# Kernel optimization log

Measured on AMD Instinct MI355X. Metric: run time of the kernel, lower is better.

Reference implementation:

```python
import jax, jax.numpy as jnp
import numpy as np

N, K, G, E, OUT = 50000, 32, 512, 400000, 8
EPS = 1e-8


def setup_inputs() -> dict:
    key = jax.random.key(0)
    ks = jax.random.split(key, 9)
    X = jax.random.uniform(ks[0], (N, G), dtype=jnp.float32)          # counts-like, non-negative
    Mu = jax.random.uniform(ks[1], (K, G), dtype=jnp.float32)
    Var = jax.random.uniform(ks[2], (K, G), dtype=jnp.float32) + 0.5  # keep variances bounded away from 0
    edge_index = jax.random.randint(ks[3], (2, E), 0, N)
    # learned parameters
    W = jax.random.normal(ks[4], (N, K), dtype=jnp.float32) * 0.1     # module inits zeros; small randn for non-trivial grads
    S = jnp.ones((N, 1), jnp.float32)
    glorot = float(np.sqrt(6.0 / (G + OUT)))
    Wl = jax.random.uniform(ks[5], (G, OUT), jnp.float32, -glorot, glorot)
    bl = jnp.zeros((OUT,), jnp.float32)
    Wr = jax.random.uniform(ks[6], (G, OUT), jnp.float32, -glorot, glorot)
    br = jnp.zeros((OUT,), jnp.float32)
    att = jax.random.normal(ks[7], (OUT,), jnp.float32) * 0.3
    return dict(X=X, Mu=Mu, Var=Var, W=W, S=S, Wl=Wl, bl=bl, Wr=Wr, br=br, att=att, edge_index=edge_index)


def reference(X, Mu, Var, W, S, Wl, bl, Wr, br, att, edge_index):
    P = jax.nn.softmax(W, axis=1)                                     # [N,K]

    # Gaussian NLL term: F[n,k] = -0.5 * sum_g (X[n,g] - Mu[k,g]*S[n])^2 / Var[k,g]
    # expanded into three GEMM-shaped contractions to avoid the [N,K,G] intermediate
    inv_var = 1.0 / Var                                               # [K,G]
    q1 = (X * X) @ inv_var.T                                          # [N,K]
    q2 = X @ (Mu * inv_var).T                                         # [N,K]
    q3 = jnp.sum(Mu * Mu * inv_var, axis=1)                           # [K]
    s = S[:, 0]                                                       # [N]
    Fmat = -0.5 * (q1 - 2.0 * s[:, None] * q2 + (s * s)[:, None] * q3[None, :])
    ll_prot = jnp.sum(P * Fmat) / X.shape[0]

    # GATv2 attention (heads=1, out=8, no self loops): only alpha is consumed downstream
    src, dst = edge_index[0], edge_index[1]
    xl = X @ Wl + bl                                                  # source transform [N,8]
    xr = X @ Wr + br                                                  # target transform [N,8]
    e = jax.nn.leaky_relu(xl[src] + xr[dst], 0.2) @ att               # [E]
    # segment softmax over edges grouped by destination node
    m = jax.lax.stop_gradient(jax.ops.segment_max(e, dst, num_segments=N))
    ex = jnp.exp(e - m[dst])
    denom = jax.ops.segment_sum(ex, dst, num_segments=N)
    alpha = ex / denom[dst]                                           # [E]

    ce_space = -jnp.sum(P[src] * alpha[:, None] * jnp.log(P[dst] + EPS)) / X.shape[0]
    return ll_prot, ce_space, P
```

## Files before the change

kernel.cpp:

```cpp
#include <hip/hip_runtime.h>
#include <hip/hip_bf16.h>
#include <math.h>

#define N_NODES 50000
#define K_COMP  32
#define G_DIM   512
#define E_EDGES 400000
#define OUT_DIM 8
#define EPSV    1e-8f

#define NPB 16
#define NB_NODE (N_NODES / NPB)
#define NB_E1   ((E_EDGES + 255) / 256)
#define NB_CE   ((E_EDGES / 2 + 255) / 256)

typedef __attribute__((ext_vector_type(8))) short short8;
typedef __attribute__((ext_vector_type(8))) unsigned short ushort8;
typedef __attribute__((ext_vector_type(4))) unsigned short ushort4v;
typedef __attribute__((ext_vector_type(4))) float f32x4;

static const size_t OFF_T    = 0;
static const size_t OFF_Q3   = OFF_T + 80 * 512;
static const size_t OFF_SRC  = OFF_Q3 + 64;
static const size_t OFF_DST  = OFF_SRC + (size_t)N_NODES * 32;
static const size_t OFF_CON  = OFF_DST + (size_t)N_NODES * 32;
static const size_t OFF_DEN  = OFF_CON + E_EDGES;
static const size_t OFF_PLL  = OFF_DEN + N_NODES;
static const size_t OFF_PCE  = OFF_PLL + 4096;

__device__ __forceinline__ unsigned short f2bf(float f) {
    __hip_bfloat16 h = __float2bfloat16(f);
    return *(unsigned short*)&h;
}
__device__ __forceinline__ float bf2f(unsigned short u) {
    unsigned v = ((unsigned)u) << 16;
    return __uint_as_float(v);
}

__global__ __launch_bounds__(256)
void prep_kernel(const float* __restrict__ Var, const float* __restrict__ Mu,
                 const float* __restrict__ Wl, const float* __restrict__ Wr,
                 unsigned short* __restrict__ Tb, float* __restrict__ den,
                 float* __restrict__ q3) {
    int idx = blockIdx.x * 256 + threadIdx.x;
    if (idx < 80 * 512) {
        int r = idx >> 9;
        int g = idx & 511;
        float v;
        if (r < 32)      v = 1.0f / Var[r * 512 + g];
        else if (r < 64) { int k = r - 32; v = Mu[k * 512 + g] / Var[k * 512 + g]; }
        else if (r < 72) { int o = r - 64; v = Wl[g * 8 + o]; }
        else             { int o = r - 72; v = Wr[g * 8 + o]; }
        int dest = ((g >> 5) * 5 + (r >> 4)) * 512 + (r & 15) * 32 + (((g & 31) >> 3) << 3) + (g & 7);
        Tb[dest] = f2bf(v);
    }
    if (idx < N_NODES) den[idx] = 0.0f;

    if (blockIdx.x < 32) {
        int k = blockIdx.x;
        int t = threadIdx.x;
        float s = 0.0f;
        for (int g = t; g < 512; g += 256) {
            float mu = Mu[k * 512 + g];
            s += mu * mu / Var[k * 512 + g];
        }
        for (int off = 32; off; off >>= 1) s += __shfl_down(s, off);
        __shared__ float sQ[4];
        if ((t & 63) == 0) sQ[t >> 6] = s;
        __syncthreads();
        if (t == 0) q3[k] = sQ[0] + sQ[1] + sQ[2] + sQ[3];
    }
}

__global__ __launch_bounds__(128, 5)
void node_kernel(const float* __restrict__ X, const float* __restrict__ W,
                 const float* __restrict__ S, const float* __restrict__ bl,
                 const float* __restrict__ br, const unsigned short* __restrict__ Tb,
                 const float* __restrict__ q3, float* __restrict__ outP,
                 float* __restrict__ srcRec, float* __restrict__ dstRec,
                 float* __restrict__ pll) {
    __shared__ float sAccH[2][NPB][81];
    __shared__ float sLL[2];

    const int t = threadIdx.x;
    const int lane = t & 63;
    const int wv = t >> 6;
    const int col = lane & 15;
    const int kg  = lane >> 4;

    const int node = blockIdx.x * NPB + col;
    const float* xrow = X + (size_t)node * 512 + wv * 256 + kg * 8;

    f32x4 acc[5];
#pragma unroll
    for (int i = 0; i < 5; ++i) acc[i] = (f32x4){0.f, 0.f, 0.f, 0.f};

    float4 v0 = *(const float4*)(xrow);
    float4 v1 = *(const float4*)(xrow + 4);

#pragma unroll
    for (int gc = 0; gc < 256; gc += 32) {
        float4 n0v, n1v;
        if (gc + 32 < 256) {
            n0v = *(const float4*)(xrow + gc + 32);
            n1v = *(const float4*)(xrow + gc + 36);
        }
        const unsigned short* bbase =
            Tb + (size_t)(wv * 8 + (gc >> 5)) * 5 * 512 + col * 32 + kg * 8;
        short8 b0 = *(const short8*)(bbase);
        short8 b1 = *(const short8*)(bbase + 512);
        short8 b2 = *(const short8*)(bbase + 1024);
        short8 b3 = *(const short8*)(bbase + 1536);
        short8 b4 = *(const short8*)(bbase + 2048);

        short8 ax, ax2;
        ax[0] = (short)f2bf(v0.x); ax[1] = (short)f2bf(v0.y);
        ax[2] = (short)f2bf(v0.z); ax[3] = (short)f2bf(v0.w);
        ax[4] = (short)f2bf(v1.x); ax[5] = (short)f2bf(v1.y);
        ax[6] = (short)f2bf(v1.z); ax[7] = (short)f2bf(v1.w);
        ax2[0] = (short)f2bf(v0.x * v0.x); ax2[1] = (short)f2bf(v0.y * v0.y);
        ax2[2] = (short)f2bf(v0.z * v0.z); ax2[3] = (short)f2bf(v0.w * v0.w);
        ax2[4] = (short)f2bf(v1.x * v1.x); ax2[5] = (short)f2bf(v1.y * v1.y);
        ax2[6] = (short)f2bf(v1.z * v1.z); ax2[7] = (short)f2bf(v1.w * v1.w);

        acc[0] = __builtin_amdgcn_mfma_f32_16x16x32_bf16(ax2, b0, acc[0], 0, 0, 0);
        acc[1] = __builtin_amdgcn_mfma_f32_16x16x32_bf16(ax2, b1, acc[1], 0, 0, 0);
        acc[2] = __builtin_amdgcn_mfma_f32_16x16x32_bf16(ax,  b2, acc[2], 0, 0, 0);
        acc[3] = __builtin_amdgcn_mfma_f32_16x16x32_bf16(ax,  b3, acc[3], 0, 0, 0);
        acc[4] = __builtin_amdgcn_mfma_f32_16x16x32_bf16(ax,  b4, acc[4], 0, 0, 0);

        v0 = n0v; v1 = n1v;
    }

#pragma unroll
    for (int tile = 0; tile < 5; ++tile)
#pragma unroll
        for (int r = 0; r < 4; ++r)
            sAccH[wv][kg * 4 + r][tile * 16 + col] = acc[tile][r];
    __syncthreads();

    const int nn = t >> 3;
    const int j = t & 7;
    const int n = blockIdx.x * NPB + nn;

    float sv = S[n];
    float sv2 = sv * sv;
    float4 wv4 = *(const float4*)(W + (size_t)n * 32 + j * 4);
    float w[4] = {wv4.x, wv4.y, wv4.z, wv4.w};
    float wm = fmaxf(fmaxf(w[0], w[1]), fmaxf(w[2], w[3]));
    wm = fmaxf(wm, __shfl_xor(wm, 1));
    wm = fmaxf(wm, __shfl_xor(wm, 2));
    wm = fmaxf(wm, __shfl_xor(wm, 4));
    float p[4], ps = 0.0f;
#pragma unroll
    for (int i = 0; i < 4; ++i) { p[i] = __expf(w[i] - wm); ps += p[i]; }
    ps += __shfl_xor(ps, 1);
    ps += __shfl_xor(ps, 2);
    ps += __shfl_xor(ps, 4);
    float inv = 1.0f / ps;

    float pv[4];
    ushort4v pb, lb;
    float ll = 0.0f;
#pragma unroll
    for (int i = 0; i < 4; ++i) {
        int k = j * 4 + i;
        float P_ = p[i] * inv;
        pv[i] = P_;
        pb[i] = f2bf(P_);
        lb[i] = f2bf(__logf(P_ + EPSV));
        float q1k = sAccH[0][nn][k] + sAccH[1][nn][k];
        float q2k = sAccH[0][nn][32 + k] + sAccH[1][nn][32 + k];
        float f = -0.5f * (q1k - 2.0f * sv * q2k + sv2 * q3[k]);
        ll = fmaf(P_, f, ll);
    }
    ll += __shfl_xor(ll, 1);
    ll += __shfl_xor(ll, 2);
    ll += __shfl_xor(ll, 4);
    float llacc = (j == 0) ? ll : 0.0f;

    size_t base = (size_t)n * 32 + j * 4;
    float2* op = (float2*)(outP + base);
    op[0] = make_float2(pv[0], pv[1]);
    op[1] = make_float2(pv[2], pv[3]);

    float* sr = srcRec + (size_t)n * 32;
    float* dr = dstRec + (size_t)n * 32;
    *(ushort4v*)&((unsigned short*)sr)[16 + j * 4] = pb;
    *(ushort4v*)&((unsigned short*)dr)[16 + j * 4] = lb;
    sr[j] = (sAccH[0][nn][64 + j] + sAccH[1][nn][64 + j]) + bl[j];
    dr[j] = (sAccH[0][nn][72 + j] + sAccH[1][nn][72 + j]) + br[j];

    for (int off = 32; off; off >>= 1) llacc += __shfl_down(llacc, off);
    if ((t & 63) == 0) sLL[wv] = llacc;
    __syncthreads();
    if (t == 0) pll[blockIdx.x] = sLL[0] + sLL[1];
}

__global__ __launch_bounds__(256, 4)
void edge1_kernel(const int* __restrict__ ei, const float* __restrict__ srcRec,
                  const float* __restrict__ dstRec, const float* __restrict__ att,
                  float* __restrict__ contrib, float* __restrict__ den) {
    int i = blockIdx.x * 256 + threadIdx.x;
    if (i >= E_EDGES) return;
    int s = ei[i];
    int d = ei[E_EDGES + i];
    const float4* sp = (const float4*)(srcRec + (size_t)s * 32);
    const float4* dp = (const float4*)(dstRec + (size_t)d * 32);
    float4 a0 = sp[0], a1 = sp[1];
    float4 b0 = dp[0], b1 = dp[1];
    const ushort8* pp = (const ushort8*)(sp + 2);
    const ushort8* lp = (const ushort8*)(dp + 2);
    ushort8 pa = pp[0], pb_ = pp[1], pc = pp[2], pd = pp[3];
    ushort8 la = lp[0], lb_ = lp[1], lc = lp[2], ld = lp[3];
    const float4* atp = (const float4*)att;
    float4 t0 = atp[0], t1 = atp[1];
    float at[8] = {t0.x, t0.y, t0.z, t0.w, t1.x, t1.y, t1.z, t1.w};
    float h[8] = {a0.x + b0.x, a0.y + b0.y, a0.z + b0.z, a0.w + b0.w,
                  a1.x + b1.x, a1.y + b1.y, a1.z + b1.z, a1.w + b1.w};
    float ev = 0.0f;
#pragma unroll
    for (int q = 0; q < 8; ++q) {
        float hv = h[q];
        hv = hv > 0.0f ? hv : 0.2f * hv;
        ev = fmaf(hv, at[q], ev);
    }
    float x = __expf(ev);
    atomicAdd(den + d, x);

    float dot = 0.0f;
#pragma unroll
    for (int r = 0; r < 8; ++r) {
        dot = fmaf(bf2f(pa[r]),  bf2f(la[r]),  dot);
        dot = fmaf(bf2f(pb_[r]), bf2f(lb_[r]), dot);
        dot = fmaf(bf2f(pc[r]),  bf2f(lc[r]),  dot);
        dot = fmaf(bf2f(pd[r]),  bf2f(ld[r]),  dot);
    }
    contrib[i] = x * dot;
}

__global__ __launch_bounds__(256, 4)
void edge2_kernel(const int* __restrict__ ei, const float* __restrict__ contrib,
                  const float* __restrict__ den, float* __restrict__ pce) {
    const int t = threadIdx.x;
    const int base = (blockIdx.x * 256 + t) * 2;
    float ce = 0.0f;
    if (base < E_EDGES) {
        int2 dd = *(const int2*)&ei[E_EDGES + base];
        float2 cv = *(const float2*)&contrib[base];
        ce = cv.x / den[dd.x] + cv.y / den[dd.y];
    }
    for (int off = 32; off; off >>= 1) ce += __shfl_down(ce, off);
    __shared__ float sC[4];
    if ((t & 63) == 0) sC[t >> 6] = ce;
    __syncthreads();
    if (t == 0) pce[blockIdx.x] = sC[0] + sC[1] + sC[2] + sC[3];
}

__global__ __launch_bounds__(256)
void finalize_kernel(const float* __restrict__ pll, const float* __restrict__ pce,
                     float* __restrict__ out) {
    const int t = threadIdx.x;
    float a = 0.0f, b = 0.0f;
    for (int i = t; i < NB_NODE; i += 256) a += pll[i];
    for (int i = t; i < NB_CE; i += 256) b += pce[i];
    for (int off = 32; off; off >>= 1) {
        a += __shfl_down(a, off);
        b += __shfl_down(b, off);
    }
    __shared__ float sA[4], sB[4];
    if ((t & 63) == 0) { sA[t >> 6] = a; sB[t >> 6] = b; }
    __syncthreads();
    if (t == 0) {
        float ll = sA[0] + sA[1] + sA[2] + sA[3];
        float ce = sB[0] + sB[1] + sB[2] + sB[3];
        out[0] = ll / (float)N_NODES;
        out[1] = -ce / (float)N_NODES;
    }
}

extern "C" void kernel_launch(void* const* d_in, const int* in_sizes, int n_in,
                              void* d_out, int out_size, void* d_ws, size_t ws_size,
                              hipStream_t stream) {
    const float* X   = (const float*)d_in[0];
    const float* Mu  = (const float*)d_in[1];
    const float* Var = (const float*)d_in[2];
    const float* W   = (const float*)d_in[3];
    const float* S   = (const float*)d_in[4];
    const float* Wl  = (const float*)d_in[5];
    const float* bl  = (const float*)d_in[6];
    const float* Wr  = (const float*)d_in[7];
    const float* br  = (const float*)d_in[8];
    const float* att = (const float*)d_in[9];
    const int*   ei  = (const int*)d_in[10];
    float* out = (float*)d_out;
    float* ws  = (float*)d_ws;

    unsigned short* Tb     = (unsigned short*)(ws + OFF_T);
    float*          q3     = ws + OFF_Q3;
    float*          srcRec = ws + OFF_SRC;
    float*          dstRec = ws + OFF_DST;
    float*          contrib= ws + OFF_CON;
    float*          den    = ws + OFF_DEN;
    float*          pll    = ws + OFF_PLL;
    float*          pce    = ws + OFF_PCE;

    prep_kernel<<<(N_NODES + 255) / 256, 256, 0, stream>>>(Var, Mu, Wl, Wr, Tb, den, q3);
    node_kernel<<<NB_NODE, 128, 0, stream>>>(X, W, S, bl, br, Tb, q3,
                                             out + 2, srcRec, dstRec, pll);
    edge1_kernel<<<NB_E1, 256, 0, stream>>>(ei, srcRec, dstRec, att, contrib, den);
    edge2_kernel<<<NB_CE, 256, 0, stream>>>(ei, contrib, den, pce);
    finalize_kernel<<<1, 256, 0, stream>>>(pll, pce, out);
}
```

Baseline: 78.51 us.

## Process 32 nodes per block with 4-way K split to reuse B fragments

The node kernel now handles 32 nodes per 256-thread block, with four waves each covering a quarter of the G dimension. Each wave computes two 16-node MFMA tiles that share the same loaded B fragments, halving B loads per node. Per-wave partial log-likelihoods are written directly, which drops the final block sync, and tail nodes are clamped and masked. The explicit software prefetch of X rows is removed, and register pressure rises from the doubled accumulators.

New measurement: 77.02 us (median of 2 runs). Within noise of the previous version (-1.9%).

```diff
diff --git a/kernel.cpp b/kernel.cpp
--- a/kernel.cpp
+++ b/kernel.cpp
@@ -9,8 +9,8 @@
 #define OUT_DIM 8
 #define EPSV    1e-8f
 
-#define NPB 16
-#define NB_NODE (N_NODES / NPB)
+#define NPB 32
+#define NB_NODE ((N_NODES + NPB - 1) / NPB)
 #define NB_E1   ((E_EDGES + 255) / 256)
 #define NB_CE   ((E_EDGES / 2 + 255) / 256)
 
@@ -26,7 +26,7 @@
 static const size_t OFF_CON  = OFF_DST + (size_t)N_NODES * 32;
 static const size_t OFF_DEN  = OFF_CON + E_EDGES;
 static const size_t OFF_PLL  = OFF_DEN + N_NODES;
-static const size_t OFF_PCE  = OFF_PLL + 4096;
+static const size_t OFF_PCE  = OFF_PLL + 8192;
 
 __device__ __forceinline__ unsigned short f2bf(float f) {
     __hip_bfloat16 h = __float2bfloat16(f);
@@ -72,80 +72,99 @@
     }
 }
 
-__global__ __launch_bounds__(128, 5)
+__global__ __launch_bounds__(256, 4)
 void node_kernel(const float* __restrict__ X, const float* __restrict__ W,
                  const float* __restrict__ S, const float* __restrict__ bl,
                  const float* __restrict__ br, const unsigned short* __restrict__ Tb,
                  const float* __restrict__ q3, float* __restrict__ outP,
                  float* __restrict__ srcRec, float* __restrict__ dstRec,
                  float* __restrict__ pll) {
-    __shared__ float sAccH[2][NPB][81];
-    __shared__ float sLL[2];
+    __shared__ float sAccH[4][NPB][80];
 
     const int t = threadIdx.x;
     const int lane = t & 63;
-    const int wv = t >> 6;
+    const int wq = t >> 6;
     const int col = lane & 15;
     const int kg  = lane >> 4;
 
-    const int node = blockIdx.x * NPB + col;
-    const float* xrow = X + (size_t)node * 512 + wv * 256 + kg * 8;
-
-    f32x4 acc[5];
-#pragma unroll
-    for (int i = 0; i < 5; ++i) acc[i] = (f32x4){0.f, 0.f, 0.f, 0.f};
-
-    float4 v0 = *(const float4*)(xrow);
-    float4 v1 = *(const float4*)(xrow + 4);
-
-#pragma unroll
-    for (int gc = 0; gc < 256; gc += 32) {
-        float4 n0v, n1v;
-        if (gc + 32 < 256) {
-            n0v = *(const float4*)(xrow + gc + 32);
-            n1v = *(const float4*)(xrow + gc + 36);
-        }
+    const int n0 = blockIdx.x * NPB;
+    int nodeA = n0 + col;
+    int nodeB = n0 + 16 + col;
+    if (nodeA >= N_NODES) nodeA = N_NODES - 1;
+    if (nodeB >= N_NODES) nodeB = N_NODES - 1;
+    const float* xrowA = X + (size_t)nodeA * 512 + wq * 128 + kg * 8;
+    const float* xrowB = X + (size_t)nodeB * 512 + wq * 128 + kg * 8;
+
+    f32x4 accA[5], accB[5];
+#pragma unroll
+    for (int i = 0; i < 5; ++i) {
+        accA[i] = (f32x4){0.f, 0.f, 0.f, 0.f};
+        accB[i] = (f32x4){0.f, 0.f, 0.f, 0.f};
+    }
+
+#pragma unroll
+    for (int it = 0; it < 4; ++it) {
         const unsigned short* bbase =
-            Tb + (size_t)(wv * 8 + (gc >> 5)) * 5 * 512 + col * 32 + kg * 8;
+            Tb + (size_t)(wq * 4 + it) * 5 * 512 + col * 32 + kg * 8;
         short8 b0 = *(const short8*)(bbase);
         short8 b1 = *(const short8*)(bbase + 512);
         short8 b2 = *(const short8*)(bbase + 1024);
         short8 b3 = *(const short8*)(bbase + 1536);
         short8 b4 = *(const short8*)(bbase + 2048);
 
-        short8 ax, ax2;
-        ax[0] = (short)f2bf(v0.x); ax[1] = (short)f2bf(v0.y);
-        ax[2] = (short)f2bf(v0.z); ax[3] = (short)f2bf(v0.w);
-        ax[4] = (short)f2bf(v1.x); ax[5] = (short)f2bf(v1.y);
-        ax[6] = (short)f2bf(v1.z); ax[7] = (short)f2bf(v1.w);
-        ax2[0] = (short)f2bf(v0.x * v0.x); ax2[1] = (short)f2bf(v0.y * v0.y);
-        ax2[2] = (short)f2bf(v0.z * v0.z); ax2[3] = (short)f2bf(v0.w * v0.w);
-        ax2[4] = (short)f2bf(v1.x * v1.x); ax2[5] = (short)f2bf(v1.y * v1.y);
-        ax2[6] = (short)f2bf(v1.z * v1.z); ax2[7] = (short)f2bf(v1.w * v1.w);
-
-        acc[0] = __builtin_amdgcn_mfma_f32_16x16x32_bf16(ax2, b0, acc[0], 0, 0, 0);
-        acc[1] = __builtin_amdgcn_mfma_f32_16x16x32_bf16(ax2, b1, acc[1], 0, 0, 0);
-        acc[2] = __builtin_amdgcn_mfma_f32_16x16x32_bf16(ax,  b2, acc[2], 0, 0, 0);
-        acc[3] = __builtin_amdgcn_mfma_f32_16x16x32_bf16(ax,  b3, acc[3], 0, 0, 0);
-        acc[4] = __builtin_amdgcn_mfma_f32_16x16x32_bf16(ax,  b4, acc[4], 0, 0, 0);
-
-        v0 = n0v; v1 = n1v;
-    }
-
-#pragma unroll
-    for (int tile = 0; tile < 5; ++tile)
-#pragma unroll
-        for (int r = 0; r < 4; ++r)
-            sAccH[wv][kg * 4 + r][tile * 16 + col] = acc[tile][r];
+        float4 va0 = *(const float4*)(xrowA + it * 32);
+        float4 va1 = *(const float4*)(xrowA + it * 32 + 4);
+        float4 vb0 = *(const float4*)(xrowB + it * 32);
+        float4 vb1 = *(const float4*)(xrowB + it * 32 + 4);
+
+        short8 axA, axA2, axB, axB2;
+        axA[0] = (short)f2bf(va0.x); axA[1] = (short)f2bf(va0.y);
+        axA[2] = (short)f2bf(va0.z); axA[3] = (short)f2bf(va0.w);
+        axA[4] = (short)f2bf(va1.x); axA[5] = (short)f2bf(va1.y);
+        axA[6] = (short)f2bf(va1.z); axA[7] = (short)f2bf(va1.w);
+        axA2[0] = (short)f2bf(va0.x * va0.x); axA2[1] = (short)f2bf(va0.y * va0.y);
+        axA2[2] = (short)f2bf(va0.z * va0.z); axA2[3] = (short)f2bf(va0.w * va0.w);
+        axA2[4] = (short)f2bf(va1.x * va1.x); axA2[5] = (short)f2bf(va1.y * va1.y);
+        axA2[6] = (short)f2bf(va1.z * va1.z); axA2[7] = (short)f2bf(va1.w * va1.w);
+        axB[0] = (short)f2bf(vb0.x); axB[1] = (short)f2bf(vb0.y);
+        axB[2] = (short)f2bf(vb0.z); axB[3] = (short)f2bf(vb0.w);
+        axB[4] = (short)f2bf(vb1.x); axB[5] = (short)f2bf(vb1.y);
+        axB[6] = (short)f2bf(vb1.z); axB[7] = (short)f2bf(vb1.w);
+        axB2[0] = (short)f2bf(vb0.x * vb0.x); axB2[1] = (short)f2bf(vb0.y * vb0.y);
+        axB2[2] = (short)f2bf(vb0.z * vb0.z); axB2[3] = (short)f2bf(vb0.w * vb0.w);
+        axB2[4] = (short)f2bf(vb1.x * vb1.x); axB2[5] = (short)f2bf(vb1.y * vb1.y);
+        axB2[6] = (short)f2bf(vb1.z * vb1.z); axB2[7] = (short)f2bf(vb1.w * vb1.w);
+
+        accA[0] = __builtin_amdgcn_mfma_f32_16x16x32_bf16(axA2, b0, accA[0], 0, 0, 0);
+        accB[0] = __builtin_amdgcn_mfma_f32_16x16x32_bf16(axB2, b0, accB[0], 0, 0, 0);
+        accA[1] = __builtin_amdgcn_mfma_f32_16x16x32_bf16(axA2, b1, accA[1], 0, 0, 0);
+        accB[1] = __builtin_amdgcn_mfma_f32_16x16x32_bf16(axB2, b1, accB[1], 0, 0, 0);
+        accA[2] = __builtin_amdgcn_mfma_f32_16x16x32_bf16(axA,  b2, accA[2], 0, 0, 0);
+        accB[2] = __builtin_amdgcn_mfma_f32_16x16x32_bf16(axB,  b2, accB[2], 0, 0, 0);
+        accA[3] = __builtin_amdgcn_mfma_f32_16x16x32_bf16(axA,  b3, accA[3], 0, 0, 0);
+        accB[3] = __builtin_amdgcn_mfma_f32_16x16x32_bf16(axB,  b3, accB[3], 0, 0, 0);
+        accA[4] = __builtin_amdgcn_mfma_f32_16x16x32_bf16(axA,  b4, accA[4], 0, 0, 0);
+        accB[4] = __builtin_amdgcn_mfma_f32_16x16x32_bf16(axB,  b4, accB[4], 0, 0, 0);
+    }
+
+#pragma unroll
+    for (int ot = 0; ot < 5; ++ot)
+#pragma unroll
+        for (int r = 0; r < 4; ++r) {
+            sAccH[wq][kg * 4 + r][ot * 16 + col]      = accA[ot][r];
+            sAccH[wq][16 + kg * 4 + r][ot * 16 + col] = accB[ot][r];
+        }
     __syncthreads();
 
     const int nn = t >> 3;
     const int j = t & 7;
-    const int n = blockIdx.x * NPB + nn;
-
-    float sv = S[n];
+    const int n = n0 + nn;
+    const bool valid = n < N_NODES;
+    const int nc = valid ? n : N_NODES - 1;
+
+    float sv = S[nc];
     float sv2 = sv * sv;
-    float4 wv4 = *(const float4*)(W + (size_t)n * 32 + j * 4);
+    float4 wv4 = *(const float4*)(W + (size_t)nc * 32 + j * 4);
     float w[4] = {wv4.x, wv4.y, wv4.z, wv4.w};
     float wm = fmaxf(fmaxf(w[0], w[1]), fmaxf(w[2], w[3]));
     wm = fmaxf(wm, __shfl_xor(wm, 1));
@@ -169,32 +188,36 @@
         pv[i] = P_;
         pb[i] = f2bf(P_);
         lb[i] = f2bf(__logf(P_ + EPSV));
-        float q1k = sAccH[0][nn][k] + sAccH[1][nn][k];
-        float q2k = sAccH[0][nn][32 + k] + sAccH[1][nn][32 + k];
+        float q1k = sAccH[0][nn][k] + sAccH[1][nn][k] +
+                    sAccH[2][nn][k] + sAccH[3][nn][k];
+        float q2k = sAccH[0][nn][32 + k] + sAccH[1][nn][32 + k] +
+                    sAccH[2][nn][32 + k] + sAccH[3][nn][32 + k];
         float f = -0.5f * (q1k - 2.0f * sv * q2k + sv2 * q3[k]);
         ll = fmaf(P_, f, ll);
     }
     ll += __shfl_xor(ll, 1);
     ll += __shfl_xor(ll, 2);
     ll += __shfl_xor(ll, 4);
-    float llacc = (j == 0) ? ll : 0.0f;
-
-    size_t base = (size_t)n * 32 + j * 4;
-    float2* op = (float2*)(outP + base);
-    op[0] = make_float2(pv[0], pv[1]);
-    op[1] = make_float2(pv[2], pv[3]);
-
-    float* sr = srcRec + (size_t)n * 32;
-    float* dr = dstRec + (size_t)n * 32;
-    *(ushort4v*)&((unsigned short*)sr)[16 + j * 4] = pb;
-    *(ushort4v*)&((unsigned short*)dr)[16 + j * 4] = lb;
-    sr[j] = (sAccH[0][nn][64 + j] + sAccH[1][nn][64 + j]) + bl[j];
-    dr[j] = (sAccH[0][nn][72 + j] + sAccH[1][nn][72 + j]) + br[j];
+    float llacc = (j == 0 && valid) ? ll : 0.0f;
+
+    if (valid) {
+        size_t base = (size_t)n * 32 + j * 4;
+        float2* op = (float2*)(outP + base);
+        op[0] = make_float2(pv[0], pv[1]);
+        op[1] = make_float2(pv[2], pv[3]);
+
+        float* sr = srcRec + (size_t)n * 32;
+        float* dr = dstRec + (size_t)n * 32;
+        *(ushort4v*)&((unsigned short*)sr)[16 + j * 4] = pb;
+        *(ushort4v*)&((unsigned short*)dr)[16 + j * 4] = lb;
+        sr[j] = (sAccH[0][nn][64 + j] + sAccH[1][nn][64 + j] +
+                 sAccH[2][nn][64 + j] + sAccH[3][nn][64 + j]) + bl[j];
+        dr[j] = (sAccH[0][nn][72 + j] + sAccH[1][nn][72 + j] +
+                 sAccH[2][nn][72 + j] + sAccH[3][nn][72 + j]) + br[j];
+    }
 
     for (int off = 32; off; off >>= 1) llacc += __shfl_down(llacc, off);
-    if ((t & 63) == 0) sLL[wv] = llacc;
-    __syncthreads();
-    if (t == 0) pll[blockIdx.x] = sLL[0] + sLL[1];
+    if (lane == 0) pll[blockIdx.x * 4 + wq] = llacc;
 }
 
 __global__ __launch_bounds__(256, 4)
@@ -262,7 +285,7 @@
                      float* __restrict__ out) {
     const int t = threadIdx.x;
     float a = 0.0f, b = 0.0f;
-    for (int i = t; i < NB_NODE; i += 256) a += pll[i];
+    for (int i = t; i < NB_NODE * 4; i += 256) a += pll[i];
     for (int i = t; i < NB_CE; i += 256) b += pce[i];
     for (int off = 32; off; off >>= 1) {
         a += __shfl_down(a, off);
@@ -306,7 +329,7 @@
     float*          pce    = ws + OFF_PCE;
 
     prep_kernel<<<(N_NODES + 255) / 256, 256, 0, stream>>>(Var, Mu, Wl, Wr, Tb, den, q3);
-    node_kernel<<<NB_NODE, 128, 0, stream>>>(X, W, S, bl, br, Tb, q3,
+    node_kernel<<<NB_NODE, 256, 0, stream>>>(X, W, S, bl, br, Tb, q3,
                                              out + 2, srcRec, dstRec, pll);
     edge1_kernel<<<NB_E1, 256, 0, stream>>>(ei, srcRec, dstRec, att, contrib, den);
     edge2_kernel<<<NB_CE, 256, 0, stream>>>(ei, contrib, den, pce);
```
